# Optimization experiments

Hardware: AMD Instinct MI355X
Metric: run time of the kernel (lower is better)

Reference implementation:

```python
import jax, jax.numpy as jnp
import numpy as np

N_NODES = 100000
N_EDGES = 1600000
NFEAT, NHID, NCLASS = 128, 64, 16


def setup_inputs() -> dict:
    key = jax.random.key(0)
    ks = jax.random.split(key, 6)
    x = jax.random.normal(ks[0], (N_NODES, NFEAT), dtype=jnp.float32)
    src = jax.random.randint(ks[1], (N_EDGES,), 0, N_NODES)
    dst = jax.random.randint(ks[2], (N_EDGES,), 0, N_NODES)
    # Glorot-ish init for the two GraphConv weights, zero bias (DGL default)
    W1 = jax.random.normal(ks[3], (NFEAT, NHID), dtype=jnp.float32) * (1.0 / np.sqrt(NFEAT))
    b1 = jnp.zeros((NHID,), dtype=jnp.float32)
    W2 = jax.random.normal(ks[4], (NHID, NCLASS), dtype=jnp.float32) * (1.0 / np.sqrt(NHID))
    b2 = jnp.zeros((NCLASS,), dtype=jnp.float32)
    return {"x": x, "src": src, "dst": dst, "W1": W1, "b1": b1, "W2": W2, "b2": b2}


def _graph_conv(h, W, b, src, dst, norm_src, norm_dst, n_nodes):
    """DGL GraphConv with norm='both': D_out^{-1/2} A D_in^{-1/2} h W + b.
    Apply W before aggregation when it reduces dimensionality (DGL's in>out path);
    the math is identical either way."""
    if W.shape[0] > W.shape[1]:
        h = h @ W
    h = h * norm_src[:, None]                                   # scale source feats
    agg = jax.ops.segment_sum(h[src], dst, num_segments=n_nodes)  # sparse A @ h
    agg = agg * norm_dst[:, None]
    if W.shape[0] <= W.shape[1]:
        agg = agg @ W
    return agg + b


def reference(x, src, dst, W1, b1, W2, b2):
    n = x.shape[0]
    ones = jnp.ones(src.shape, dtype=x.dtype)
    out_deg = jax.ops.segment_sum(ones, src, num_segments=n)
    in_deg = jax.ops.segment_sum(ones, dst, num_segments=n)
    norm_src = jnp.maximum(out_deg, 1.0) ** -0.5  # degree clamp as in DGL
    norm_dst = jnp.maximum(in_deg, 1.0) ** -0.5
    h = jax.nn.relu(_graph_conv(x, W1, b1, src, dst, norm_src, norm_dst, n))
    # dropout: p=0 / eval mode -> identity
    h = _graph_conv(h, W2, b2, src, dst, norm_src, norm_dst, n)
    return jax.nn.log_softmax(h, axis=1)
```

## Files before the change

### kernel.cpp

```cpp
#include <hip/hip_runtime.h>
#include <hip/hip_bf16.h>

#define NN 100000
#define NE 1600000
#define NF 128
#define NH 64
#define NC 16
#define NB1 391
#define GBIN 256
#define CHUNK 6250
#define BBUK 196
#define NCB 196
#define NGRP 1563

typedef __attribute__((ext_vector_type(8))) short short8v;
typedef __attribute__((ext_vector_type(4))) float float4v;

__device__ __forceinline__ float us2f(unsigned short u) {
    return __uint_as_float(((unsigned int)u) << 16);
}
__device__ __forceinline__ float bflo(unsigned u) {
    return __uint_as_float(u << 16);
}
__device__ __forceinline__ float bfhi(unsigned u) {
    return __uint_as_float(u & 0xFFFF0000u);
}
__device__ __forceinline__ unsigned short f2us_rn(float f) {
    unsigned int u = __float_as_uint(f);
    return (unsigned short)((u + 0x7FFFu + ((u >> 16) & 1u)) >> 16);
}
__device__ __forceinline__ float ldf(const void* p, size_t i, bool f32) {
    return f32 ? ((const float*)p)[i] : us2f(((const unsigned short*)p)[i]);
}

__global__ void k_sniffprep(const unsigned short* __restrict__ xu,
                            const void* __restrict__ W1,
                            unsigned short* __restrict__ W1f,
                            int* __restrict__ mode) {
    __shared__ int cnt;
    if (threadIdx.x == 0) cnt = 0;
    __syncthreads();
    int c = 0;
    for (int i = threadIdx.x; i < 4096; i += 256) {
        unsigned int e = (xu[i] >> 7) & 0xFFu;
        if (e >= 160u) c++;
    }
    atomicAdd(&cnt, c);
    __syncthreads();
    if (threadIdx.x == 0) mode[0] = (cnt >= 16) ? 1 : 0;
    __syncthreads();
    const bool f32 = (cnt >= 16);
    for (int i = threadIdx.x; i < 1024; i += 256) {
        const int kcnt = i >> 6, lane = i & 63;
        const int kc = kcnt >> 2, nt = kcnt & 3;
        const int quad = lane >> 4, col = lane & 15;
        #pragma unroll
        for (int j = 0; j < 8; ++j) {
            const size_t idx = (size_t)(kc * 32 + quad * 8 + j) * NH + nt * 16 + col;
            W1f[(size_t)i * 8 + j] = f32 ? f2us_rn(((const float*)W1)[idx])
                                         : ((const unsigned short*)W1)[idx];
        }
    }
}

__global__ void k_deg(const int4* __restrict__ src4, const int4* __restrict__ dst4,
                      int* __restrict__ deg_out, int* __restrict__ deg_in) {
    int i = blockIdx.x * blockDim.x + threadIdx.x;
    if (i < NE / 4) {
        int4 s = src4[i], d = dst4[i];
        atomicAdd(&deg_out[s.x], 1); atomicAdd(&deg_out[s.y], 1);
        atomicAdd(&deg_out[s.z], 1); atomicAdd(&deg_out[s.w], 1);
        atomicAdd(&deg_in[d.x], 1);  atomicAdd(&deg_in[d.y], 1);
        atomicAdd(&deg_in[d.z], 1);  atomicAdd(&deg_in[d.w], 1);
    }
}

__global__ void k_scatter(const int* __restrict__ src, const int* __restrict__ dst,
                          int* __restrict__ cursor, int* __restrict__ srcs_sorted) {
    int e = blockIdx.x * blockDim.x + threadIdx.x;
    if (e < NE) {
        int p = atomicAdd(&cursor[dst[e]], 1);
        srcs_sorted[p] = src[e];
    }
}

__global__ void k_scan_a(const int* __restrict__ deg_in, int* __restrict__ bsum) {
    __shared__ int s[256];
    int i = blockIdx.x * 256 + threadIdx.x;
    s[threadIdx.x] = (i < NN) ? deg_in[i] : 0;
    __syncthreads();
    for (int off = 128; off > 0; off >>= 1) {
        if (threadIdx.x < off) s[threadIdx.x] += s[threadIdx.x + off];
        __syncthreads();
    }
    if (threadIdx.x == 0) bsum[blockIdx.x] = s[0];
}

__global__ void k_scan_b(const int* __restrict__ bsum, int* __restrict__ boff) {
    __shared__ int s[512];
    int t = threadIdx.x;
    s[t] = (t < NB1) ? bsum[t] : 0;
    __syncthreads();
    for (int off = 1; off < 512; off <<= 1) {
        int v = (t >= off) ? s[t - off] : 0;
        __syncthreads();
        s[t] += v;
        __syncthreads();
    }
    if (t < NB1) boff[t] = (t == 0) ? 0 : s[t - 1];
}

__global__ void k_scan_c(const int* __restrict__ deg_in, const int* __restrict__ deg_out,
                         const int* __restrict__ boff, int* __restrict__ row_off,
                         int* __restrict__ cursor, float* __restrict__ nsrc,
                         float* __restrict__ ndst) {
    __shared__ int s[256];
    int t = threadIdx.x;
    int i = blockIdx.x * 256 + t;
    int d = (i < NN) ? deg_in[i] : 0;
    s[t] = d;
    __syncthreads();
    for (int off = 1; off < 256; off <<= 1) {
        int v = (t >= off) ? s[t - off] : 0;
        __syncthreads();
        s[t] += v;
        __syncthreads();
    }
    int excl = s[t] - d + boff[blockIdx.x];
    if (i < NN) {
        row_off[i] = excl;
        cursor[i]  = excl;
        ndst[i] = rsqrtf(fmaxf((float)d, 1.0f));
        nsrc[i] = rsqrtf(fmaxf((float)deg_out[i], 1.0f));
        if (i == NN - 1) row_off[NN] = excl + d;
    }
}

__global__ __launch_bounds__(256) void k_hist2(const int* __restrict__ src,
                                               const int* __restrict__ dst,
                                               int* __restrict__ counts_d,
                                               int* __restrict__ counts_s) {
    __shared__ int hd[BBUK], hs[BBUK];
    for (int i = threadIdx.x; i < BBUK; i += 256) { hd[i] = 0; hs[i] = 0; }
    __syncthreads();
    const int g = blockIdx.x;
    const int e0 = g * CHUNK;
    for (int i = threadIdx.x; i < CHUNK; i += 256) {
        atomicAdd(&hd[dst[e0 + i] >> 9], 1);
        atomicAdd(&hs[src[e0 + i] >> 9], 1);
    }
    __syncthreads();
    for (int i = threadIdx.x; i < BBUK; i += 256) {
        counts_d[i * GBIN + g] = hd[i];
        counts_s[i * GBIN + g] = hs[i];
    }
}

__global__ void k_cs_a(const int* __restrict__ counts, int* __restrict__ csum) {
    __shared__ int s[256];
    int i = blockIdx.x * 256 + threadIdx.x;
    s[threadIdx.x] = counts[i];
    __syncthreads();
    for (int off = 128; off > 0; off >>= 1) {
        if (threadIdx.x < off) s[threadIdx.x] += s[threadIdx.x + off];
        __syncthreads();
    }
    if (threadIdx.x == 0) csum[blockIdx.x] = s[0];
}

__global__ void k_cs_b2(const int* __restrict__ csum, int* __restrict__ coff) {
    __shared__ int s[512];
    int t = threadIdx.x;
    int half = t >> 8, j = t & 255;
    s[t] = (j < NCB) ? csum[half * NCB + j] : 0;
    __syncthreads();
    for (int off = 1; off < 256; off <<= 1) {
        int v = (j >= off) ? s[t - off] : 0;
        __syncthreads();
        s[t] += v;
        __syncthreads();
    }
    if (j < NCB) coff[half * NCB + j] = (j == 0) ? 0 : s[t - 1];
}

__global__ void k_cs_c(int* __restrict__ counts, const int* __restrict__ coff) {
    __shared__ int s[256];
    int t = threadIdx.x;
    int i = blockIdx.x * 256 + t;
    int v = counts[i];
    s[t] = v;
    __syncthreads();
    for (int off = 1; off < 256; off <<= 1) {
        int u = (t >= off) ? s[t - off] : 0;
        __syncthreads();
        s[t] += u;
        __syncthreads();
    }
    counts[i] = s[t] - v + coff[blockIdx.x];
}

__global__ __launch_bounds__(256) void k_binscatter2(const int* __restrict__ src,
                                                     const int* __restrict__ dst,
                                                     const int* __restrict__ counts_d,
                                                     const int* __restrict__ counts_s,
                                                     unsigned int* __restrict__ packed,
                                                     unsigned short* __restrict__ packed2) {
    __shared__ int curd[BBUK], curs[BBUK];
    const int g = blockIdx.x;
    for (int i = threadIdx.x; i < BBUK; i += 256) {
        curd[i] = counts_d[i * GBIN + g];
        curs[i] = counts_s[i * GBIN + g];
    }
    __syncthreads();
    const int e0 = g * CHUNK;
    for (int i = threadIdx.x; i < CHUNK; i += 256) {
        int s = src[e0 + i], d = dst[e0 + i];
        int pd = atomicAdd(&curd[d >> 9], 1);
        packed[pd] = ((unsigned)s << 9) | (unsigned)(d & 511);
        int ps = atomicAdd(&curs[s >> 9], 1);
        packed2[ps] = (unsigned short)(s & 511);
    }
}

__global__ __launch_bounds__(256) void k_bucket2(const int* __restrict__ counts_d,
                                                 const int* __restrict__ counts_s,
                                                 const unsigned int* __restrict__ packed,
                                                 const unsigned short* __restrict__ packed2,
                                                 int* __restrict__ row_off,
                                                 float* __restrict__ ndst,
                                                 float* __restrict__ nsrc,
                                                 int* __restrict__ srcs_sorted) {
    __shared__ int h[512];
    const int b = blockIdx.x;
    const int n0 = b << 9;
    const int nlim = (NN - n0 < 512) ? (NN - n0) : 512;
    const int t = threadIdx.x;

    for (int j = t; j < 512; j += 256) h[j] = 0;
    __syncthreads();
    {
        const int sbeg = counts_s[b * GBIN];
        const int send = (b + 1 < BBUK) ? counts_s[(b + 1) * GBIN] : NE;
        for (int i = sbeg + t; i < send; i += 256)
            atomicAdd(&h[packed2[i] & 511u], 1);
    }
    __syncthreads();
    for (int j = t; j < nlim; j += 256)
        nsrc[n0 + j] = rsqrtf(fmaxf((float)h[j], 1.0f));
    __syncthreads();

    for (int j = t; j < 512; j += 256) h[j] = 0;
    __syncthreads();
    const int beg = counts_d[b * GBIN];
    const int end = (b + 1 < BBUK) ? counts_d[(b + 1) * GBIN] : NE;
    for (int i = beg + t; i < end; i += 256)
        atomicAdd(&h[packed[i] & 511u], 1);
    __syncthreads();
    const int degA = h[t], degB = h[t + 256];
    int offset = 1;
    #pragma unroll
    for (int d = 256; d > 0; d >>= 1) {
        __syncthreads();
        if (t < d) {
            int ai = offset * (2 * t + 1) - 1;
            int bi = offset * (2 * t + 2) - 1;
            h[bi] += h[ai];
        }
        offset <<= 1;
    }
    __syncthreads();
    if (t == 0) h[511] = 0;
    #pragma unroll
    for (int d = 1; d < 512; d <<= 1) {
        offset >>= 1;
        __syncthreads();
        if (t < d) {
            int ai = offset * (2 * t + 1) - 1;
            int bi = offset * (2 * t + 2) - 1;
            int tmp = h[ai]; h[ai] = h[bi]; h[bi] += tmp;
        }
    }
    __syncthreads();
    const int r0 = beg + h[t];
    const int r1 = beg + h[t + 256];
    if (t < nlim) {
        row_off[n0 + t] = r0;
        ndst[n0 + t] = rsqrtf(fmaxf((float)degA, 1.0f));
    }
    if (t + 256 < nlim) {
        row_off[n0 + t + 256] = r1;
        ndst[n0 + t + 256] = rsqrtf(fmaxf((float)degB, 1.0f));
    }
    if (n0 + nlim == NN && t == 0) row_off[NN] = end;
    __syncthreads();
    h[t] = r0; h[t + 256] = r1;
    __syncthreads();
    for (int i = beg + t; i < end; i += 256) {
        unsigned v = packed[i];
        int p = atomicAdd(&h[v & 511u], 1);
        srcs_sorted[p] = (int)(v >> 9);
    }
}

__global__ __launch_bounds__(256) void k_gemm1_mfma(
    const void* __restrict__ x, const unsigned short* __restrict__ W1f,
    const float* __restrict__ nsrc, unsigned short* __restrict__ h1,
    const int* __restrict__ mode)
{
    const bool f32 = (mode[0] != 0);
    const int tid = threadIdx.x;
    const int wave = tid >> 6, lane = tid & 63;
    const int col = lane & 15, quad = lane >> 4;

    short8v bfrag[16];
    #pragma unroll
    for (int f = 0; f < 16; ++f)
        bfrag[f] = *(const short8v*)(W1f + ((size_t)f * 64 + lane) * 8);

    const int base = blockIdx.x * 64 + wave * 16;
    int arow = base + col;
    if (arow > NN - 1) arow = NN - 1;

    short8v afrag[4];
    if (f32) {
        const float4* ap = (const float4*)((const float*)x + (size_t)arow * NF);
        #pragma unroll
        for (int kc = 0; kc < 4; ++kc) {
            float4 v0 = ap[kc * 8 + quad * 2];
            float4 v1 = ap[kc * 8 + quad * 2 + 1];
            short8v af;
            af[0] = (short)f2us_rn(v0.x); af[1] = (short)f2us_rn(v0.y);
            af[2] = (short)f2us_rn(v0.z); af[3] = (short)f2us_rn(v0.w);
            af[4] = (short)f2us_rn(v1.x); af[5] = (short)f2us_rn(v1.y);
            af[6] = (short)f2us_rn(v1.z); af[7] = (short)f2us_rn(v1.w);
            afrag[kc] = af;
        }
    } else {
        const uint4* ap = (const uint4*)((const unsigned short*)x + (size_t)arow * NF);
        #pragma unroll
        for (int kc = 0; kc < 4; ++kc) {
            uint4 v = ap[kc * 4 + quad];
            afrag[kc] = *reinterpret_cast<const short8v*>(&v);
        }
    }

    float4v acc[4];
    #pragma unroll
    for (int nt = 0; nt < 4; ++nt) acc[nt] = (float4v){0.f, 0.f, 0.f, 0.f};
    #pragma unroll
    for (int kc = 0; kc < 4; ++kc)
        #pragma unroll
        for (int nt = 0; nt < 4; ++nt)
            acc[nt] = __builtin_amdgcn_mfma_f32_16x16x32_bf16(afrag[kc], bfrag[kc * 4 + nt], acc[nt], 0, 0, 0);

    #pragma unroll
    for (int reg = 0; reg < 4; ++reg) {
        const int row = base + quad * 4 + reg;
        if (row < NN) {
            const float ns = nsrc[row];
            unsigned short* hp = h1 + (size_t)row * NH + col;
            hp[0]  = f2us_rn(acc[0][reg] * ns);
            hp[16] = f2us_rn(acc[1][reg] * ns);
            hp[32] = f2us_rn(acc[2][reg] * ns);
            hp[48] = f2us_rn(acc[3][reg] * ns);
        }
    }
}

__global__ __launch_bounds__(256) void k_agg1csr(
    const int* __restrict__ row_off, const int* __restrict__ srcs,
    const unsigned short* __restrict__ h1, const float* __restrict__ ndst,
    const float* __restrict__ nsrc, const void* __restrict__ b1,
    const void* __restrict__ W2, const int* __restrict__ mode,
    unsigned short* __restrict__ h2)
{
    const bool f32 = (mode[0] != 0);
    const int lane = threadIdx.x & 63;
    const int q  = lane >> 4;
    const int li = lane & 15;

    const float bias0 = ldf(b1, 4*li+0, f32), bias1 = ldf(b1, 4*li+1, f32);
    const float bias2 = ldf(b1, 4*li+2, f32), bias3 = ldf(b1, 4*li+3, f32);
    float w2[4][4];
    #pragma unroll
    for (int j = 0; j < 4; ++j)
        #pragma unroll
        for (int m = 0; m < 4; ++m)
            w2[j][m] = ldf(W2, (size_t)(4*li+j)*NC + (q + 4*m), f32);

    const int wid = (blockIdx.x * blockDim.x + threadIdx.x) >> 6;
    const int nw  = (gridDim.x * blockDim.x) >> 6;
    const uint2* __restrict__ h1v = (const uint2*)h1;
    const unsigned uli = (unsigned)li;

    int row = wid;
    if (row >= NN) return;
    int beg = row_off[row];
    int end = row_off[row + 1];
    float nd = ndst[row];
    float ns = nsrc[row];

    while (row < NN) {
        const int nrow = row + nw;
        int nbeg = 0, nend = 0;
        float nnd = 0.f, nns = 0.f;
        if (nrow < NN) {
            nbeg = row_off[nrow];
            nend = row_off[nrow + 1];
            nnd  = ndst[nrow];
            nns  = nsrc[nrow];
        }

        float ax = 0.f, ay = 0.f, az = 0.f, aw = 0.f;
        float bx = 0.f, by = 0.f, bz = 0.f, bw = 0.f;
        const int e1 = end - 1;
        int i = beg + q;
        while (i < end) {
            const int j1 = i + 4, j2 = i + 8, j3 = i + 12;
            const int t1 = (j1 < end) ? j1 : e1;
            const int t2 = (j2 < end) ? j2 : e1;
            const int t3 = (j3 < end) ? j3 : e1;
            const int s0 = srcs[(unsigned)i];
            const int s1 = srcs[(unsigned)t1];
            const int s2 = srcs[(unsigned)t2];
            const int s3 = srcs[(unsigned)t3];
            const uint2 v0 = h1v[(unsigned)s0 * 16u + uli];
            const uint2 v1 = h1v[(unsigned)s1 * 16u + uli];
            const uint2 v2 = h1v[(unsigned)s2 * 16u + uli];
            const uint2 v3 = h1v[(unsigned)s3 * 16u + uli];
            ax += bflo(v0.x); ay += bfhi(v0.x);
            az += bflo(v0.y); aw += bfhi(v0.y);
            if (j1 < end) {
                bx += bflo(v1.x); by += bfhi(v1.x);
                bz += bflo(v1.y); bw += bfhi(v1.y);
            }
            if (j2 < end) {
                ax += bflo(v2.x); ay += bfhi(v2.x);
                az += bflo(v2.y); aw += bfhi(v2.y);
            }
            if (j3 < end) {
                bx += bflo(v3.x); by += bfhi(v3.x);
                bz += bflo(v3.y); bw += bfhi(v3.y);
            }
            i += 16;
        }
        ax += bx; ay += by; az += bz; aw += bw;
        ax += __shfl_xor(ax, 16); ay += __shfl_xor(ay, 16);
        az += __shfl_xor(az, 16); aw += __shfl_xor(aw, 16);
        ax += __shfl_xor(ax, 32); ay += __shfl_xor(ay, 32);
        az += __shfl_xor(az, 32); aw += __shfl_xor(aw, 32);

        const float t0 = fmaxf(fmaf(ax, nd, bias0), 0.f);
        const float t1f = fmaxf(fmaf(ay, nd, bias1), 0.f);
        const float t2f = fmaxf(fmaf(az, nd, bias2), 0.f);
        const float t3f = fmaxf(fmaf(aw, nd, bias3), 0.f);

        float p0 = fmaf(t0,w2[0][0],fmaf(t1f,w2[1][0],fmaf(t2f,w2[2][0],t3f*w2[3][0])));
        float p1 = fmaf(t0,w2[0][1],fmaf(t1f,w2[1][1],fmaf(t2f,w2[2][1],t3f*w2[3][1])));
        float p2 = fmaf(t0,w2[0][2],fmaf(t1f,w2[1][2],fmaf(t2f,w2[2][2],t3f*w2[3][2])));
        float p3 = fmaf(t0,w2[0][3],fmaf(t1f,w2[1][3],fmaf(t2f,w2[2][3],t3f*w2[3][3])));
        #pragma unroll
        for (int off = 1; off <= 8; off <<= 1) {
            p0 += __shfl_xor(p0, off);
            p1 += __shfl_xor(p1, off);
            p2 += __shfl_xor(p2, off);
            p3 += __shfl_xor(p3, off);
        }
        if (li < 4) {
            float v = (li == 0) ? p0 : (li == 1) ? p1 : (li == 2) ? p2 : p3;
            h2[(size_t)row * NC + q + 4*li] = f2us_rn(v * ns);
        }

        row = nrow; beg = nbeg; end = nend; nd = nnd; ns = nns;
    }
}

__global__ __launch_bounds__(256) void k_out(
    const int* __restrict__ row_off, const int* __restrict__ srcs,
    const unsigned short* __restrict__ h2, const float* __restrict__ ndst,
    const void* __restrict__ b2, const int* __restrict__ mode,
    void* __restrict__ out)
{
    const bool f32 = (mode[0] != 0);
    const int lane = threadIdx.x & 63;
    const int q  = lane >> 3;
    const int li = lane & 7;
    const float b2v0 = ldf(b2, 2*li,   f32);
    const float b2v1 = ldf(b2, 2*li+1, f32);

    const int wid = (blockIdx.x * blockDim.x + threadIdx.x) >> 6;
    const int nw  = (gridDim.x * blockDim.x) >> 6;
    const unsigned* __restrict__ h2v = (const unsigned*)h2;
    const unsigned uli = (unsigned)li;

    int row = wid;
    if (row >= NN) return;
    int beg = row_off[row];
    int end = row_off[row + 1];
    float nd = ndst[row];

    while (row < NN) {
        const int nrow = row + nw;
        int nbeg = 0, nend = 0;
        float nnd = 0.f;
        if (nrow < NN) {
            nbeg = row_off[nrow];
            nend = row_off[nrow + 1];
            nnd  = ndst[nrow];
        }

        float a0 = 0.f, a1 = 0.f, c0 = 0.f, c1 = 0.f;
        const int e1 = end - 1;
        int i = beg + q;
        while (i < end) {
            const int j1 = i + 8;
            const int t1 = (j1 < end) ? j1 : e1;
            const int s0 = srcs[(unsigned)i];
            const int s1 = srcs[(unsigned)t1];
            const unsigned u0 = h2v[(unsigned)s0 * 8u + uli];
            const unsigned u1 = h2v[(unsigned)s1 * 8u + uli];
            a0 += bflo(u0); a1 += bfhi(u0);
            if (j1 < end) {
                c0 += bflo(u1); c1 += bfhi(u1);
            }
            i += 16;
        }
        a0 += c0; a1 += c1;
        #pragma unroll
        for (int off = 8; off <= 32; off <<= 1) {
            a0 += __shfl_xor(a0, off);
            a1 += __shfl_xor(a1, off);
        }
        float v0 = fmaf(a0, nd, b2v0);
        float v1 = fmaf(a1, nd, b2v1);
        float m = fmaxf(v0, v1);
        #pragma unroll
        for (int off = 1; off <= 4; off <<= 1) m = fmaxf(m, __shfl_xor(m, off));
        float sm = __expf(v0 - m) + __expf(v1 - m);
        #pragma unroll
        for (int off = 1; off <= 4; off <<= 1) sm += __shfl_xor(sm, off);
        const float lsm = __logf(sm);
        const float r0 = v0 - m - lsm, r1 = v1 - m - lsm;
        if (q == 0) {
            if (f32) {
                float2 o; o.x = r0; o.y = r1;
                *(float2*)((float*)out + (size_t)row * NC + 2*li) = o;
            } else {
                unsigned o = ((unsigned)f2us_rn(r1) << 16) | (unsigned)f2us_rn(r0);
                *(unsigned*)((unsigned short*)out + (size_t)row * NC + 2*li) = o;
            }
        }

        row = nrow; beg = nbeg; end = nend; nd = nnd;
    }
}

extern "C" void kernel_launch(void* const* d_in, const int* in_sizes, int n_in,
                              void* d_out, int out_size, void* d_ws, size_t ws_size,
                              hipStream_t stream) {
    const void* x  = d_in[0];
    const int* src = (const int*)d_in[1];
    const int* dst = (const int*)d_in[2];
    const void* W1 = d_in[3];
    const void* b1 = d_in[4];
    const void* W2 = d_in[5];
    const void* b2 = d_in[6];

    char* ws = (char*)d_ws;
    const size_t O_MODE = 0;
    const size_t O_W1F  = 1024;
    const size_t O_CNT  = O_W1F + 16384;
    const size_t O_CS   = O_CNT  + 401408;
    const size_t O_DEG  = O_CS   + 4096;
    const size_t O_NSRC = O_DEG  + 800000;
    const size_t O_NDST = O_NSRC + 400000;
    const size_t O_ROW  = O_NDST + 400000;
    const size_t O_CUR  = O_ROW  + 400128;
    const size_t O_BS   = O_CUR  + 400128;
    const size_t O_SRCS = O_BS   + 4096;
    const size_t O_H2   = O_SRCS + 6400000;
    const size_t O_H1   = O_H2   + 3200000;
    const size_t NEED = O_H1 + 12800000;
    const bool fast_csr = ws_size >= NEED;

    int*   mode     = (int*)(ws + O_MODE);
    unsigned short* W1f = (unsigned short*)(ws + O_W1F);
    int*   counts_d = (int*)(ws + O_CNT);
    int*   counts_s = counts_d + BBUK * GBIN;
    int*   csum     = (int*)(ws + O_CS);
    int*   coff     = (int*)(ws + O_CS + 2048);
    int*   deg_out  = (int*)(ws + O_DEG);
    int*   deg_in   = deg_out + NN;
    float* nsrc     = (float*)(ws + O_NSRC);
    float* ndst     = (float*)(ws + O_NDST);
    int*   row_off  = (int*)(ws + O_ROW);
    int*   cursor   = (int*)(ws + O_CUR);
    int*   bsum     = (int*)(ws + O_BS);
    int*   boff     = (int*)(ws + O_BS + 2048);
    int*   srcs_s   = (int*)(ws + O_SRCS);
    unsigned short* h2 = (unsigned short*)(ws + O_H2);
    unsigned short* h1 = (unsigned short*)(ws + O_H1);
    unsigned int*   packed  = (unsigned int*)(ws + O_H1);
    unsigned short* packed2 = (unsigned short*)(ws + O_H1 + 6400000);

    k_sniffprep<<<1, 256, 0, stream>>>((const unsigned short*)x, W1, W1f, mode);
    if (fast_csr) {
        k_hist2<<<GBIN, 256, 0, stream>>>(src, dst, counts_d, counts_s);
        k_cs_a<<<2 * NCB, 256, 0, stream>>>(counts_d, csum);
        k_cs_b2<<<1, 512, 0, stream>>>(csum, coff);
        k_cs_c<<<2 * NCB, 256, 0, stream>>>(counts_d, coff);
        k_binscatter2<<<GBIN, 256, 0, stream>>>(src, dst, counts_d, counts_s, packed, packed2);
        k_bucket2<<<BBUK, 256, 0, stream>>>(counts_d, counts_s, packed, packed2,
                                            row_off, ndst, nsrc, srcs_s);
    } else {
        hipMemsetAsync(deg_out, 0, 2 * (size_t)NN * sizeof(int), stream);
        k_deg<<<(NE / 4 + 255) / 256, 256, 0, stream>>>((const int4*)src, (const int4*)dst, deg_out, deg_in);
        k_scan_a<<<NB1, 256, 0, stream>>>(deg_in, bsum);
        k_scan_b<<<1, 512, 0, stream>>>(bsum, boff);
        k_scan_c<<<NB1, 256, 0, stream>>>(deg_in, deg_out, boff, row_off, cursor, nsrc, ndst);
        k_scatter<<<(NE + 255) / 256, 256, 0, stream>>>(src, dst, cursor, srcs_s);
    }
    k_gemm1_mfma<<<NGRP, 256, 0, stream>>>(x, W1f, nsrc, h1, mode);
    k_agg1csr<<<2048, 256, 0, stream>>>(row_off, srcs_s, h1, ndst, nsrc, b1, W2, mode, h2);
    k_out<<<2048, 256, 0, stream>>>(row_off, srcs_s, h2, ndst, b2, mode, d_out);
}
```

Measured before the change: 275.7 us.

## Fold sniff/W1 prep into histogram kernel and drop separate block-offset scan

The standalone dtype-sniff and W1 repack kernel becomes an extra block of the histogram kernel, and the single-block scan k_cs_b2 is removed by having each k_cs_c block reduce the preceding csum entries itself. Together these cut two kernel launches from the CSR build chain. The histogram, binscatter and bucket kernels also move to 512-thread blocks, so k_bucket2 handles one node per thread. The cost is redundant prefix reductions in every k_cs_c block and a different occupancy profile for the CSR kernels.

```diff
diff --git a/kernel.cpp b/kernel.cpp
--- a/kernel.cpp
+++ b/kernel.cpp
@@ -136,21 +136,53 @@
     }
 }
 
-__global__ __launch_bounds__(256) void k_hist2(const int* __restrict__ src,
-                                               const int* __restrict__ dst,
-                                               int* __restrict__ counts_d,
-                                               int* __restrict__ counts_s) {
+__global__ __launch_bounds__(512) void k_hist2s(const int* __restrict__ src,
+                                                const int* __restrict__ dst,
+                                                int* __restrict__ counts_d,
+                                                int* __restrict__ counts_s,
+                                                const unsigned short* __restrict__ xu,
+                                                const void* __restrict__ W1,
+                                                unsigned short* __restrict__ W1f,
+                                                int* __restrict__ mode) {
     __shared__ int hd[BBUK], hs[BBUK];
-    for (int i = threadIdx.x; i < BBUK; i += 256) { hd[i] = 0; hs[i] = 0; }
+    __shared__ int cnt;
+    const int t = threadIdx.x;
+    if (blockIdx.x == GBIN) {
+        if (t == 0) cnt = 0;
+        __syncthreads();
+        int c = 0;
+        for (int i = t; i < 4096; i += 512) {
+            unsigned int e = (xu[i] >> 7) & 0xFFu;
+            if (e >= 160u) c++;
+        }
+        atomicAdd(&cnt, c);
+        __syncthreads();
+        if (t == 0) mode[0] = (cnt >= 16) ? 1 : 0;
+        __syncthreads();
+        const bool f32 = (cnt >= 16);
+        for (int i = t; i < 1024; i += 512) {
+            const int kcnt = i >> 6, lane = i & 63;
+            const int kc = kcnt >> 2, nt = kcnt & 3;
+            const int quad = lane >> 4, col = lane & 15;
+            #pragma unroll
+            for (int j = 0; j < 8; ++j) {
+                const size_t idx = (size_t)(kc * 32 + quad * 8 + j) * NH + nt * 16 + col;
+                W1f[(size_t)i * 8 + j] = f32 ? f2us_rn(((const float*)W1)[idx])
+                                             : ((const unsigned short*)W1)[idx];
+            }
+        }
+        return;
+    }
+    for (int i = t; i < BBUK; i += 512) { hd[i] = 0; hs[i] = 0; }
     __syncthreads();
     const int g = blockIdx.x;
     const int e0 = g * CHUNK;
-    for (int i = threadIdx.x; i < CHUNK; i += 256) {
+    for (int i = t; i < CHUNK; i += 512) {
         atomicAdd(&hd[dst[e0 + i] >> 9], 1);
         atomicAdd(&hs[src[e0 + i] >> 9], 1);
     }
     __syncthreads();
-    for (int i = threadIdx.x; i < BBUK; i += 256) {
+    for (int i = t; i < BBUK; i += 512) {
         counts_d[i * GBIN + g] = hd[i];
         counts_s[i * GBIN + g] = hs[i];
     }
@@ -168,26 +200,22 @@
     if (threadIdx.x == 0) csum[blockIdx.x] = s[0];
 }
 
-__global__ void k_cs_b2(const int* __restrict__ csum, int* __restrict__ coff) {
-    __shared__ int s[512];
-    int t = threadIdx.x;
-    int half = t >> 8, j = t & 255;
-    s[t] = (j < NCB) ? csum[half * NCB + j] : 0;
-    __syncthreads();
-    for (int off = 1; off < 256; off <<= 1) {
-        int v = (j >= off) ? s[t - off] : 0;
-        __syncthreads();
-        s[t] += v;
-        __syncthreads();
-    }
-    if (j < NCB) coff[half * NCB + j] = (j == 0) ? 0 : s[t - 1];
-}
-
-__global__ void k_cs_c(int* __restrict__ counts, const int* __restrict__ coff) {
+__global__ void k_cs_c(int* __restrict__ counts, const int* __restrict__ csum) {
     __shared__ int s[256];
-    int t = threadIdx.x;
-    int i = blockIdx.x * 256 + t;
-    int v = counts[i];
+    const int t = threadIdx.x;
+    const int blk = blockIdx.x;
+    const int half = (blk >= NCB) ? 1 : 0;
+    const int j = blk - half * NCB;
+    s[t] = (t < j) ? csum[half * NCB + t] : 0;
+    __syncthreads();
+    for (int off = 128; off > 0; off >>= 1) {
+        if (t < off) s[t] += s[t + off];
+        __syncthreads();
+    }
+    const int blockoff = s[0];
+    __syncthreads();
+    const int i = blk * 256 + t;
+    const int v = counts[i];
     s[t] = v;
     __syncthreads();
     for (int off = 1; off < 256; off <<= 1) {
@@ -196,24 +224,25 @@
         s[t] += u;
         __syncthreads();
     }
-    counts[i] = s[t] - v + coff[blockIdx.x];
-}
-
-__global__ __launch_bounds__(256) void k_binscatter2(const int* __restrict__ src,
+    counts[i] = s[t] - v + blockoff;
+}
+
+__global__ __launch_bounds__(512) void k_binscatter2(const int* __restrict__ src,
                                                      const int* __restrict__ dst,
                                                      const int* __restrict__ counts_d,
                                                      const int* __restrict__ counts_s,
                                                      unsigned int* __restrict__ packed,
                                                      unsigned short* __restrict__ packed2) {
     __shared__ int curd[BBUK], curs[BBUK];
+    const int t = threadIdx.x;
     const int g = blockIdx.x;
-    for (int i = threadIdx.x; i < BBUK; i += 256) {
+    for (int i = t; i < BBUK; i += 512) {
         curd[i] = counts_d[i * GBIN + g];
         curs[i] = counts_s[i * GBIN + g];
     }
     __syncthreads();
     const int e0 = g * CHUNK;
-    for (int i = threadIdx.x; i < CHUNK; i += 256) {
+    for (int i = t; i < CHUNK; i += 512) {
         int s = src[e0 + i], d = dst[e0 + i];
         int pd = atomicAdd(&curd[d >> 9], 1);
         packed[pd] = ((unsigned)s << 9) | (unsigned)(d & 511);
@@ -222,7 +251,7 @@
     }
 }
 
-__global__ __launch_bounds__(256) void k_bucket2(const int* __restrict__ counts_d,
+__global__ __launch_bounds__(512) void k_bucket2(const int* __restrict__ counts_d,
                                                  const int* __restrict__ counts_s,
                                                  const unsigned int* __restrict__ packed,
                                                  const unsigned short* __restrict__ packed2,
@@ -236,27 +265,26 @@
     const int nlim = (NN - n0 < 512) ? (NN - n0) : 512;
     const int t = threadIdx.x;
 
-    for (int j = t; j < 512; j += 256) h[j] = 0;
+    h[t] = 0;
     __syncthreads();
     {
         const int sbeg = counts_s[b * GBIN];
         const int send = (b + 1 < BBUK) ? counts_s[(b + 1) * GBIN] : NE;
-        for (int i = sbeg + t; i < send; i += 256)
+        for (int i = sbeg + t; i < send; i += 512)
             atomicAdd(&h[packed2[i] & 511u], 1);
     }
     __syncthreads();
-    for (int j = t; j < nlim; j += 256)
-        nsrc[n0 + j] = rsqrtf(fmaxf((float)h[j], 1.0f));
-    __syncthreads();
-
-    for (int j = t; j < 512; j += 256) h[j] = 0;
+    if (t < nlim) nsrc[n0 + t] = rsqrtf(fmaxf((float)h[t], 1.0f));
+    __syncthreads();
+
+    h[t] = 0;
     __syncthreads();
     const int beg = counts_d[b * GBIN];
     const int end = (b + 1 < BBUK) ? counts_d[(b + 1) * GBIN] : NE;
-    for (int i = beg + t; i < end; i += 256)
+    for (int i = beg + t; i < end; i += 512)
         atomicAdd(&h[packed[i] & 511u], 1);
     __syncthreads();
-    const int degA = h[t], degB = h[t + 256];
+    const int deg = h[t];
     int offset = 1;
     #pragma unroll
     for (int d = 256; d > 0; d >>= 1) {
@@ -282,20 +310,15 @@
     }
     __syncthreads();
     const int r0 = beg + h[t];
-    const int r1 = beg + h[t + 256];
     if (t < nlim) {
         row_off[n0 + t] = r0;
-        ndst[n0 + t] = rsqrtf(fmaxf((float)degA, 1.0f));
-    }
-    if (t + 256 < nlim) {
-        row_off[n0 + t + 256] = r1;
-        ndst[n0 + t + 256] = rsqrtf(fmaxf((float)degB, 1.0f));
+        ndst[n0 + t] = rsqrtf(fmaxf((float)deg, 1.0f));
     }
     if (n0 + nlim == NN && t == 0) row_off[NN] = end;
     __syncthreads();
-    h[t] = r0; h[t + 256] = r1;
-    __syncthreads();
-    for (int i = beg + t; i < end; i += 256) {
+    h[t] = r0;
+    __syncthreads();
+    for (int i = beg + t; i < end; i += 512) {
         unsigned v = packed[i];
         int p = atomicAdd(&h[v & 511u], 1);
         srcs_sorted[p] = (int)(v >> 9);
@@ -603,16 +626,16 @@
     unsigned int*   packed  = (unsigned int*)(ws + O_H1);
     unsigned short* packed2 = (unsigned short*)(ws + O_H1 + 6400000);
 
-    k_sniffprep<<<1, 256, 0, stream>>>((const unsigned short*)x, W1, W1f, mode);
     if (fast_csr) {
-        k_hist2<<<GBIN, 256, 0, stream>>>(src, dst, counts_d, counts_s);
+        k_hist2s<<<GBIN + 1, 512, 0, stream>>>(src, dst, counts_d, counts_s,
+                                               (const unsigned short*)x, W1, W1f, mode);
         k_cs_a<<<2 * NCB, 256, 0, stream>>>(counts_d, csum);
-        k_cs_b2<<<1, 512, 0, stream>>>(csum, coff);
-        k_cs_c<<<2 * NCB, 256, 0, stream>>>(counts_d, coff);
-        k_binscatter2<<<GBIN, 256, 0, stream>>>(src, dst, counts_d, counts_s, packed, packed2);
-        k_bucket2<<<BBUK, 256, 0, stream>>>(counts_d, counts_s, packed, packed2,
+        k_cs_c<<<2 * NCB, 256, 0, stream>>>(counts_d, csum);
+        k_binscatter2<<<GBIN, 512, 0, stream>>>(src, dst, counts_d, counts_s, packed, packed2);
+        k_bucket2<<<BBUK, 512, 0, stream>>>(counts_d, counts_s, packed, packed2,
                                             row_off, ndst, nsrc, srcs_s);
     } else {
+        k_sniffprep<<<1, 256, 0, stream>>>((const unsigned short*)x, W1, W1f, mode);
         hipMemsetAsync(deg_out, 0, 2 * (size_t)NN * sizeof(int), stream);
         k_deg<<<(NE / 4 + 255) / 256, 256, 0, stream>>>((const int4*)src, (const int4*)dst, deg_out, deg_in);
         k_scan_a<<<NB1, 256, 0, stream>>>(deg_in, bsum);
```

After: 244.2 us. -11.4%, faster.
